# Kernel tuning notes

Measured on AMD Instinct MI355X. Metric: run time of the kernel, lower is better.

The kernel has to match this reference:

```python
import jax, jax.numpy as jnp
from jax import lax
import numpy as np

B, P, M1, M2, M3 = 128, 168, 2, 2, 2
M = M1 * M2 * M3
HIDC, HIDR, HIDS, CK, SKIP, HW = 50, 50, 5, 6, 24, 24
PT = (P - CK) // SKIP  # int((P-Ck)/skip) = 6
L = P - CK + 1         # 163


def gru(xs, w_ih, w_hh, b_ih, b_hh, hid):
    # xs: [T, N, in]; torch nn.GRU cell semantics, h0 = 0. Returns final h: [N, hid].
    def step(h, x):
        gi = x @ w_ih.T + b_ih
        gh = h @ w_hh.T + b_hh
        ir, iz, inn = jnp.split(gi, 3, axis=-1)
        hr, hz, hn = jnp.split(gh, 3, axis=-1)
        r = jax.nn.sigmoid(ir + hr)
        z = jax.nn.sigmoid(iz + hz)
        n = jnp.tanh(inn + r * hn)
        return (1.0 - z) * n + z * h, None
    h0 = jnp.zeros((xs.shape[1], hid), xs.dtype)
    h, _ = lax.scan(step, h0, xs)
    return h


def setup_inputs() -> dict:
    key = jax.random.key(0)
    ks = jax.random.split(key, 16)
    O = P * HIDC * CK  # 50400 conv output channels
    d = {
        'x': jax.random.normal(ks[0], (B, P, M1, M2, M3), jnp.float32),
        'conv_w': jax.random.normal(ks[1], (O, P, M1, M2, M3), jnp.float32) * 0.02,
        'conv_b': jax.random.normal(ks[2], (O,), jnp.float32) * 0.02,
        'g1_wih': jax.random.normal(ks[3], (3 * HIDR, HIDC), jnp.float32) * 0.1,
        'g1_whh': jax.random.normal(ks[4], (3 * HIDR, HIDR), jnp.float32) * 0.1,
        'g1_bih': jax.random.normal(ks[5], (3 * HIDR,), jnp.float32) * 0.1,
        'g1_bhh': jax.random.normal(ks[6], (3 * HIDR,), jnp.float32) * 0.1,
        'gs_wih': jax.random.normal(ks[7], (3 * HIDS, HIDC), jnp.float32) * 0.1,
        'gs_whh': jax.random.normal(ks[8], (3 * HIDS, HIDS), jnp.float32) * 0.1,
        'gs_bih': jax.random.normal(ks[9], (3 * HIDS,), jnp.float32) * 0.1,
        'gs_bhh': jax.random.normal(ks[10], (3 * HIDS,), jnp.float32) * 0.1,
        'l1_w': jax.random.normal(ks[11], (M, HIDR + SKIP * HIDS), jnp.float32) * 0.1,
        'l1_b': jax.random.normal(ks[12], (M,), jnp.float32) * 0.1,
        'hw_w': jax.random.normal(ks[13], (1, HW), jnp.float32) * 0.1,
        'hw_b': jax.random.normal(ks[14], (1,), jnp.float32) * 0.1,
    }
    return d


def reference(x, conv_w, conv_b, g1_wih, g1_whh, g1_bih, g1_bhh,
              gs_wih, gs_whh, gs_bih, gs_bhh, l1_w, l1_b, hw_w, hw_b):
    # Conv3d with kernel == full spatial extent is a dense matmul over (P*m1*m2*m3).
    xf = x.reshape(B, -1)                       # [B, P*M]
    wf = conv_w.reshape(conv_w.shape[0], -1)    # [O, P*M]
    c = jax.nn.relu(xf @ wf.T + conv_b)         # [B, O]
    c = c.reshape(B, HIDC, CK, P)
    # Diagonal strided sum (the torch triple loop): res1[b,c,t] = sum_k c[b,c,k,k+t]
    res1 = sum(c[:, :, k, k:k + L] for k in range(CK))  # [B, HIDC, L]
    # dropout: eval mode (identity)
    r = gru(jnp.transpose(res1, (2, 0, 1)), g1_wih, g1_whh, g1_bih, g1_bhh, HIDR)  # [B, HIDR]
    # skip GRU
    s = res1[:, :, -PT * SKIP:]                          # [B, HIDC, PT*SKIP]
    s = s.reshape(B, HIDC, PT, SKIP)
    s = jnp.transpose(s, (2, 0, 3, 1)).reshape(PT, B * SKIP, HIDC)
    hs = gru(s, gs_wih, gs_whh, gs_bih, gs_bhh, HIDS)    # [B*SKIP, HIDS]
    hs = hs.reshape(B, SKIP * HIDS)
    r = jnp.concatenate([r, hs], axis=1)                 # [B, HIDR + SKIP*HIDS]
    res = r @ l1_w.T + l1_b                              # [B, M]
    # highway (AR) component over the last HW timesteps
    z = x[:, -HW:].reshape(B, HW, M)                     # [B, HW, M]
    z = jnp.transpose(z, (0, 2, 1)).reshape(-1, HW)      # [B*M, HW]
    z = z @ hw_w.T + hw_b                                # [B*M, 1]
    res = res + z.reshape(B, M)
    res = jax.nn.sigmoid(res)
    return res.reshape(B, M1, M2, M3)
```

## Files before the change

kernel.cpp:

```cpp
#include <hip/hip_runtime.h>
#include <hip/hip_bf16.h>
#include <cstdint>


typedef __attribute__((ext_vector_type(8))) short short8;
typedef __attribute__((ext_vector_type(4))) float f32x4;

__device__ __forceinline__ unsigned short bf16rn(float f) {
    unsigned u = __float_as_uint(f);
    return (unsigned short)((u + 0x7FFFu + ((u >> 16) & 1u)) >> 16);
}
__device__ __forceinline__ unsigned pk2(float a, float b) {
    return ((unsigned)bf16rn(b) << 16) | (unsigned)bf16rn(a);
}
__device__ __forceinline__ uint4 pack8(float4 f0, float4 f1) {
    uint4 u;
    u.x = pk2(f0.x, f0.y); u.y = pk2(f0.z, f0.w);
    u.z = pk2(f1.x, f1.y); u.w = pk2(f1.z, f1.w);
    return u;
}
__device__ __forceinline__ float bf2f(unsigned short u) {
    return __uint_as_float((unsigned)u << 16);
}
__device__ __forceinline__ float sigmf(float x) { return 1.f / (1.f + __expf(-x)); }
__device__ __forceinline__ float tanhf_(float x) { return 1.f - 2.f / (__expf(2.f * x) + 1.f); }

__global__ __launch_bounds__(256, 2)
void k1_conv_gemm(const float* __restrict__ x, const float* __restrict__ w,
                  const float* __restrict__ bias, unsigned short* __restrict__ c) {
    __shared__ uint4 a_lds[8 * 129];
    __shared__ uint4 b_lds[8 * 113];
    const int tid  = threadIdx.x;
    const int n0   = blockIdx.x * 112;
    const int wave = tid >> 6, lane = tid & 63;
    const int quad = lane >> 4, m16 = lane & 15;

    f32x4 acc[2][7];
#pragma unroll
    for (int i = 0; i < 2; ++i)
#pragma unroll
        for (int j = 0; j < 7; ++j) acc[i][j] = (f32x4){0.f, 0.f, 0.f, 0.f};

    float4 pa[4][2];
    float4 pb[4][2];

    auto issue = [&](int kb) {
#pragma unroll
        for (int i = 0; i < 4; ++i) {
            int row = (tid >> 3) + 32 * i;
            const float* gp = x + row * 1344 + kb + (tid & 7) * 8;
            pa[i][0] = *reinterpret_cast<const float4*>(gp);
            pa[i][1] = *reinterpret_cast<const float4*>(gp + 4);
        }
#pragma unroll
        for (int i = 0; i < 4; ++i) {
            int idx = tid + 256 * i;
            if (idx < 896) {
                int row = idx >> 3;
                const float* gp = w + (size_t)(n0 + row) * 1344 + kb + (idx & 7) * 8;
                pb[i][0] = *reinterpret_cast<const float4*>(gp);
                pb[i][1] = *reinterpret_cast<const float4*>(gp + 4);
            }
        }
    };

    issue(0);
    for (int kb = 0; kb < 1344; kb += 64) {
#pragma unroll
        for (int i = 0; i < 4; ++i) {
            int idx = tid + 256 * i;
            int row = idx >> 3, ks = idx & 7;
            a_lds[ks * 129 + row] = pack8(pa[i][0], pa[i][1]);
        }
#pragma unroll
        for (int i = 0; i < 4; ++i) {
            int idx = tid + 256 * i;
            if (idx < 896) {
                int row = idx >> 3, ks = idx & 7;
                b_lds[ks * 113 + row] = pack8(pb[i][0], pb[i][1]);
            }
        }
        __syncthreads();
        if (kb + 64 < 1344) issue(kb + 64);
#pragma unroll
        for (int half = 0; half < 2; ++half) {
            const int kp = half * 4 + quad;
            short8 af[2], bfr[7];
#pragma unroll
            for (int rt = 0; rt < 2; ++rt)
                af[rt] = ((const short8*)a_lds)[kp * 129 + wave * 32 + rt * 16 + m16];
#pragma unroll
            for (int ct = 0; ct < 7; ++ct)
                bfr[ct] = ((const short8*)b_lds)[kp * 113 + ct * 16 + m16];
#pragma unroll
            for (int rt = 0; rt < 2; ++rt)
#pragma unroll
                for (int ct = 0; ct < 7; ++ct)
                    acc[rt][ct] = __builtin_amdgcn_mfma_f32_16x16x32_bf16(
                        af[rt], bfr[ct], acc[rt][ct], 0, 0, 0);
        }
        __syncthreads();
    }
#pragma unroll
    for (int ct = 0; ct < 7; ++ct) {
        int col = n0 + ct * 16 + m16;
        float bv = bias[col];
#pragma unroll
        for (int rt = 0; rt < 2; ++rt) {
#pragma unroll
            for (int r = 0; r < 4; ++r) {
                int grow = wave * 32 + rt * 16 + quad * 4 + r;
                float v = acc[rt][ct][r] + bv;
                v = fmaxf(v, 0.f);
                c[(size_t)grow * 50400 + col] = bf16rn(v);
            }
        }
    }
}

__global__ __launch_bounds__(384, 1)
void k_fused(const unsigned short* __restrict__ c,
             const float* __restrict__ g1_wih, const float* __restrict__ g1_whh,
             const float* __restrict__ g1_bih, const float* __restrict__ g1_bhh,
             const float* __restrict__ gs_wih, const float* __restrict__ gs_whh,
             const float* __restrict__ gs_bih, const float* __restrict__ gs_bhh,
             const float* __restrict__ l1_w, const float* __restrict__ l1_b,
             const float* __restrict__ x, const float* __restrict__ hw_w,
             const float* __restrict__ hw_b, float* __restrict__ out) {
    __shared__ float rloc[50 * 164];
    __shared__ float gi1l[163 * 150];
    __shared__ float gi2l[144 * 15];
    __shared__ float l1wl[8 * 170];
    __shared__ __align__(16) float hl[2][64];
    __shared__ float hsl[120];
    __shared__ float r1l[64];

    const int b    = blockIdx.x;
    const int tid  = threadIdx.x;
    const int wave = tid >> 6, lane = tid & 63;

    const unsigned short* cb = c + (size_t)b * 50400;
    for (int idx = tid; idx < 8150; idx += 384) {
        int hc = idx / 163, t = idx - hc * 163;
        int base = hc * 1008 + t;
        float s = 0.f;
#pragma unroll
        for (int k = 0; k < 6; ++k) s += bf2f(cb[base + 169 * k]);
        rloc[hc * 164 + t] = s;
    }
    for (int idx = tid; idx < 1360; idx += 384) l1wl[idx] = l1_w[idx];
    __syncthreads();

    {
        const int tB   = (wave >> 1) * 64 + lane;
        const int half = wave & 1;
        if (tB < 163) {
            float xcol[50];
#pragma unroll
            for (int j = 0; j < 50; ++j) xcol[j] = rloc[j * 164 + tB];

            const int c0 = __builtin_amdgcn_readfirstlane(half * 75);
            const float* wbase = g1_wih + c0 * 50;
            float* gdst = &gi1l[tB * 150 + c0];
            for (int cc = 0; cc < 75; ++cc) {
                const float* wp = wbase + cc * 50;
                float acc = g1_bih[c0 + cc];
#pragma unroll
                for (int j = 0; j < 50; ++j) acc += xcol[j] * wp[j];
                gdst[cc] = acc;
            }
            if (tB >= 19) {
                const int r2 = tB - 19;
                const int d0 = __builtin_amdgcn_readfirstlane(half * 8);
                const int ncol = half ? 7 : 8;
                float* g2 = &gi2l[r2 * 15];
                for (int cc = 0; cc < ncol; ++cc) {
                    const float* wp = gs_wih + (d0 + cc) * 50;
                    float acc = gs_bih[d0 + cc];
#pragma unroll
                    for (int j = 0; j < 50; ++j) acc += xcol[j] * wp[j];
                    g2[d0 + cc] = acc;
                }
            }
        }
    }
    __syncthreads();

    float wr[50], wz[50], wn[50];
    float bhr = 0.f, bhz = 0.f, bhn = 0.f, hcur = 0.f;
    int lc = 0;
    float* wl1 = rloc;
    if (wave == 0) {
        for (int idx = lane; idx < 7500; idx += 64) wl1[idx] = g1_whh[idx];
        hl[0][lane] = 0.f;
        hl[1][lane] = 0.f;
        lc = (lane < 50) ? lane : 49;
#pragma unroll
        for (int j = 0; j < 50; ++j) {
            wr[j] = wl1[lc * 50 + j];
            wz[j] = wl1[(50 + lc) * 50 + j];
            wn[j] = wl1[(100 + lc) * 50 + j];
        }
        bhr = g1_bhh[lc]; bhz = g1_bhh[50 + lc]; bhn = g1_bhh[100 + lc];
    }
    float h2[5] = {0.f, 0.f, 0.f, 0.f, 0.f};

    int p = 0;
    for (int t = 0; t < 163; ++t) {
        if (wave == 0) {
            float gir = gi1l[t * 150 + lc];
            float giz = gi1l[t * 150 + 50 + lc];
            float gin = gi1l[t * 150 + 100 + lc];
            const float* hp = hl[p];
            float ar = bhr, az = bhz, an = bhn;
#pragma unroll
            for (int j4 = 0; j4 < 12; ++j4) {
                float4 hv = *reinterpret_cast<const float4*>(hp + 4 * j4);
                ar += wr[4 * j4 + 0] * hv.x + wr[4 * j4 + 1] * hv.y +
                      wr[4 * j4 + 2] * hv.z + wr[4 * j4 + 3] * hv.w;
                az += wz[4 * j4 + 0] * hv.x + wz[4 * j4 + 1] * hv.y +
                      wz[4 * j4 + 2] * hv.z + wz[4 * j4 + 3] * hv.w;
                an += wn[4 * j4 + 0] * hv.x + wn[4 * j4 + 1] * hv.y +
                      wn[4 * j4 + 2] * hv.z + wn[4 * j4 + 3] * hv.w;
            }
            {
                float h48 = hp[48], h49 = hp[49];
                ar += wr[48] * h48 + wr[49] * h49;
                az += wz[48] * h48 + wz[49] * h49;
                an += wn[48] * h48 + wn[49] * h49;
            }
            float rg = sigmf(gir + ar);
            float zg = sigmf(giz + az);
            float ng = tanhf_(gin + rg * an);
            float hn = (1.f - zg) * ng + zg * hcur;
            hl[1 - p][lane] = hn;
            hcur = hn;
        } else if (wave == 1 && t < 6 && lane < 24) {
            const float* gp = &gi2l[(t * 24 + lane) * 15];
            float gi[15];
#pragma unroll
            for (int i = 0; i < 15; ++i) gi[i] = gp[i];
            float gh[15];
#pragma unroll
            for (int i = 0; i < 15; ++i) {
                float s = gs_bhh[i];
#pragma unroll
                for (int j = 0; j < 5; ++j) s += gs_whh[i * 5 + j] * h2[j];
                gh[i] = s;
            }
#pragma unroll
            for (int u = 0; u < 5; ++u) {
                float rg = sigmf(gi[u] + gh[u]);
                float zg = sigmf(gi[5 + u] + gh[5 + u]);
                float ng = tanhf_(gi[10 + u] + rg * gh[10 + u]);
                h2[u] = (1.f - zg) * ng + zg * h2[u];
            }
        }
        __syncthreads();
        p ^= 1;
    }
    if (wave == 0 && lane < 50) r1l[lane] = hcur;
    if (wave == 1 && lane < 24) {
#pragma unroll
        for (int u = 0; u < 5; ++u) hsl[lane * 5 + u] = h2[u];
    }
    __syncthreads();

    if (tid < 8) {
        const int m = tid;
        float acc = l1_b[m];
        const float* wrow = &l1wl[m * 170];
#pragma unroll
        for (int j = 0; j < 50; ++j) acc += r1l[j] * wrow[j];
#pragma unroll
        for (int j = 0; j < 120; ++j) acc += hsl[j] * wrow[50 + j];
        float z = hw_b[0];
        const float* xb = x + (size_t)b * 1344 + 144 * 8 + m;
#pragma unroll
        for (int wi = 0; wi < 24; ++wi) z += xb[wi * 8] * hw_w[wi];
        out[b * 8 + m] = 1.f / (1.f + __expf(-(acc + z)));
    }
}

extern "C" void kernel_launch(void* const* d_in, const int* in_sizes, int n_in,
                              void* d_out, int out_size, void* d_ws, size_t ws_size,
                              hipStream_t stream) {
    const float* x      = (const float*)d_in[0];
    const float* conv_w = (const float*)d_in[1];
    const float* conv_b = (const float*)d_in[2];
    const float* g1_wih = (const float*)d_in[3];
    const float* g1_whh = (const float*)d_in[4];
    const float* g1_bih = (const float*)d_in[5];
    const float* g1_bhh = (const float*)d_in[6];
    const float* gs_wih = (const float*)d_in[7];
    const float* gs_whh = (const float*)d_in[8];
    const float* gs_bih = (const float*)d_in[9];
    const float* gs_bhh = (const float*)d_in[10];
    const float* l1_w   = (const float*)d_in[11];
    const float* l1_b   = (const float*)d_in[12];
    const float* hw_w   = (const float*)d_in[13];
    const float* hw_b   = (const float*)d_in[14];
    float* out = (float*)d_out;

    unsigned short* c = (unsigned short*)d_ws;

    hipLaunchKernelGGL(k1_conv_gemm, dim3(450), dim3(256), 0, stream, x, conv_w, conv_b, c);
    hipLaunchKernelGGL(k_fused,      dim3(128), dim3(384), 0, stream,
                       c, g1_wih, g1_whh, g1_bih, g1_bhh,
                       gs_wih, gs_whh, gs_bih, gs_bhh,
                       l1_w, l1_b, x, hw_w, hw_b, out);
}
```

Before: 566.5 us.

## Run GRU recurrence on a single wave without block barriers, packed FMA

After the input projections, all waves except wave 0 exit, and wave 0 runs the 163-step main GRU using a single shared hidden buffer with no __syncthreads per step. The small skip GRU and the final linear/highway output are then computed serially by the same wave. Recurrent weights are loaded directly from global into f32x2 registers to allow packed FMA, and sigmoid/tanh use the hardware rcp instead of a division. The intent is to cut per-step block-wide barrier latency and ALU cost on the serial critical path. It relies on wave-synchronous execution for correctness of the single-buffered hidden state and approximates the reciprocal.

```diff
diff --git a/kernel.cpp b/kernel.cpp
--- a/kernel.cpp
+++ b/kernel.cpp
@@ -5,6 +5,7 @@
 
 typedef __attribute__((ext_vector_type(8))) short short8;
 typedef __attribute__((ext_vector_type(4))) float f32x4;
+typedef __attribute__((ext_vector_type(2))) float f32x2;
 
 __device__ __forceinline__ unsigned short bf16rn(float f) {
     unsigned u = __float_as_uint(f);
@@ -22,8 +23,12 @@
 __device__ __forceinline__ float bf2f(unsigned short u) {
     return __uint_as_float((unsigned)u << 16);
 }
-__device__ __forceinline__ float sigmf(float x) { return 1.f / (1.f + __expf(-x)); }
-__device__ __forceinline__ float tanhf_(float x) { return 1.f - 2.f / (__expf(2.f * x) + 1.f); }
+__device__ __forceinline__ float sigmf(float x) {
+    return __builtin_amdgcn_rcpf(1.f + __expf(-x));
+}
+__device__ __forceinline__ float tanhf_(float x) {
+    return 1.f - 2.f * __builtin_amdgcn_rcpf(__expf(2.f * x) + 1.f);
+}
 
 __global__ __launch_bounds__(256, 2)
 void k1_conv_gemm(const float* __restrict__ x, const float* __restrict__ w,
@@ -131,9 +136,9 @@
     __shared__ float gi1l[163 * 150];
     __shared__ float gi2l[144 * 15];
     __shared__ float l1wl[8 * 170];
-    __shared__ __align__(16) float hl[2][64];
+    __shared__ __align__(16) float hl[64];
     __shared__ float hsl[120];
-    __shared__ float r1l[64];
+    __shared__ float r1l[50];
 
     const int b    = blockIdx.x;
     const int tid  = threadIdx.x;
@@ -185,61 +190,64 @@
         }
     }
     __syncthreads();
-
-    float wr[50], wz[50], wn[50];
-    float bhr = 0.f, bhz = 0.f, bhn = 0.f, hcur = 0.f;
-    int lc = 0;
-    float* wl1 = rloc;
-    if (wave == 0) {
-        for (int idx = lane; idx < 7500; idx += 64) wl1[idx] = g1_whh[idx];
-        hl[0][lane] = 0.f;
-        hl[1][lane] = 0.f;
-        lc = (lane < 50) ? lane : 49;
-#pragma unroll
-        for (int j = 0; j < 50; ++j) {
-            wr[j] = wl1[lc * 50 + j];
-            wz[j] = wl1[(50 + lc) * 50 + j];
-            wn[j] = wl1[(100 + lc) * 50 + j];
-        }
-        bhr = g1_bhh[lc]; bhz = g1_bhh[50 + lc]; bhn = g1_bhh[100 + lc];
-    }
-    float h2[5] = {0.f, 0.f, 0.f, 0.f, 0.f};
-
-    int p = 0;
+    if (wave != 0) return;
+
+    const int lc = (lane < 50) ? lane : 49;
+    f32x2 wr2[25], wz2[25], wn2[25];
+    {
+        const float* wrp = g1_whh + lc * 50;
+        const float* wzp = g1_whh + (50 + lc) * 50;
+        const float* wnp = g1_whh + (100 + lc) * 50;
+#pragma unroll
+        for (int j = 0; j < 25; ++j) {
+            wr2[j] = *reinterpret_cast<const f32x2*>(wrp + 2 * j);
+            wz2[j] = *reinterpret_cast<const f32x2*>(wzp + 2 * j);
+            wn2[j] = *reinterpret_cast<const f32x2*>(wnp + 2 * j);
+        }
+#pragma unroll
+        for (int j = 0; j < 25; ++j) {
+            asm volatile("" : "+v"(wr2[j]));
+            asm volatile("" : "+v"(wz2[j]));
+            asm volatile("" : "+v"(wn2[j]));
+        }
+    }
+    const float bhr = g1_bhh[lc], bhz = g1_bhh[50 + lc], bhn = g1_bhh[100 + lc];
+    hl[lane] = 0.f;
+    float hcur = 0.f;
+    const float* gp = gi1l;
     for (int t = 0; t < 163; ++t) {
-        if (wave == 0) {
-            float gir = gi1l[t * 150 + lc];
-            float giz = gi1l[t * 150 + 50 + lc];
-            float gin = gi1l[t * 150 + 100 + lc];
-            const float* hp = hl[p];
-            float ar = bhr, az = bhz, an = bhn;
-#pragma unroll
-            for (int j4 = 0; j4 < 12; ++j4) {
-                float4 hv = *reinterpret_cast<const float4*>(hp + 4 * j4);
-                ar += wr[4 * j4 + 0] * hv.x + wr[4 * j4 + 1] * hv.y +
-                      wr[4 * j4 + 2] * hv.z + wr[4 * j4 + 3] * hv.w;
-                az += wz[4 * j4 + 0] * hv.x + wz[4 * j4 + 1] * hv.y +
-                      wz[4 * j4 + 2] * hv.z + wz[4 * j4 + 3] * hv.w;
-                an += wn[4 * j4 + 0] * hv.x + wn[4 * j4 + 1] * hv.y +
-                      wn[4 * j4 + 2] * hv.z + wn[4 * j4 + 3] * hv.w;
-            }
-            {
-                float h48 = hp[48], h49 = hp[49];
-                ar += wr[48] * h48 + wr[49] * h49;
-                az += wz[48] * h48 + wz[49] * h49;
-                an += wn[48] * h48 + wn[49] * h49;
-            }
-            float rg = sigmf(gir + ar);
-            float zg = sigmf(giz + az);
-            float ng = tanhf_(gin + rg * an);
-            float hn = (1.f - zg) * ng + zg * hcur;
-            hl[1 - p][lane] = hn;
-            hcur = hn;
-        } else if (wave == 1 && t < 6 && lane < 24) {
-            const float* gp = &gi2l[(t * 24 + lane) * 15];
+        float gir = gp[lc], giz = gp[50 + lc], gin = gp[100 + lc];
+        float4 h4[12];
+#pragma unroll
+        for (int j4 = 0; j4 < 12; ++j4)
+            h4[j4] = *reinterpret_cast<const float4*>(&hl[4 * j4]);
+        f32x2 ht; ht.x = hl[48]; ht.y = hl[49];
+        f32x2 ar = {0.f, 0.f}, az = {0.f, 0.f}, an = {0.f, 0.f};
+#pragma unroll
+        for (int j4 = 0; j4 < 12; ++j4) {
+            f32x2 h0; h0.x = h4[j4].x; h0.y = h4[j4].y;
+            f32x2 h1; h1.x = h4[j4].z; h1.y = h4[j4].w;
+            ar += wr2[2 * j4] * h0; ar += wr2[2 * j4 + 1] * h1;
+            az += wz2[2 * j4] * h0; az += wz2[2 * j4 + 1] * h1;
+            an += wn2[2 * j4] * h0; an += wn2[2 * j4 + 1] * h1;
+        }
+        ar += wr2[24] * ht; az += wz2[24] * ht; an += wn2[24] * ht;
+        float rg = sigmf(gir + bhr + ar.x + ar.y);
+        float zg = sigmf(giz + bhz + az.x + az.y);
+        float ng = tanhf_(gin + rg * (bhn + an.x + an.y));
+        hcur = (1.f - zg) * ng + zg * hcur;
+        hl[lane] = hcur;
+        gp += 150;
+    }
+    if (lane < 50) r1l[lane] = hcur;
+
+    if (lane < 24) {
+        float h2[5] = {0.f, 0.f, 0.f, 0.f, 0.f};
+        for (int pt = 0; pt < 6; ++pt) {
+            const float* g2 = &gi2l[(pt * 24 + lane) * 15];
             float gi[15];
 #pragma unroll
-            for (int i = 0; i < 15; ++i) gi[i] = gp[i];
+            for (int i = 0; i < 15; ++i) gi[i] = g2[i];
             float gh[15];
 #pragma unroll
             for (int i = 0; i < 15; ++i) {
@@ -256,18 +264,12 @@
                 h2[u] = (1.f - zg) * ng + zg * h2[u];
             }
         }
-        __syncthreads();
-        p ^= 1;
-    }
-    if (wave == 0 && lane < 50) r1l[lane] = hcur;
-    if (wave == 1 && lane < 24) {
 #pragma unroll
         for (int u = 0; u < 5; ++u) hsl[lane * 5 + u] = h2[u];
     }
-    __syncthreads();
-
-    if (tid < 8) {
-        const int m = tid;
+
+    if (lane < 8) {
+        const int m = lane;
         float acc = l1_b[m];
         const float* wrow = &l1wl[m * 170];
 #pragma unroll
@@ -278,7 +280,7 @@
         const float* xb = x + (size_t)b * 1344 + 144 * 8 + m;
 #pragma unroll
         for (int wi = 0; wi < 24; ++wi) z += xb[wi * 8] * hw_w[wi];
-        out[b * 8 + m] = 1.f / (1.f + __expf(-(acc + z)));
+        out[b * 8 + m] = __builtin_amdgcn_rcpf(1.f + __expf(-(acc + z)));
     }
 }
 
```

New measurement: 510.5 us. 1.11x faster.
